# Optimization experiments

Measured on AMD Instinct MI355X. Metric: run time of the kernel, lower is better.

Reference implementation:

```python
import jax, jax.numpy as jnp
import numpy as np

NDIR = 6      # build_tree.num_directions()
IDIM = 256
ODIM = 512
B, L, NCH = 8, 4096, 8192


def setup_inputs() -> dict:
    key = jax.random.key(0)
    ks = jax.random.split(key, 9)
    last = jax.random.normal(ks[0], (B, NCH, IDIM), dtype=jnp.float32)
    child_l = jax.random.randint(ks[1], (L,), 0, NCH, dtype=jnp.int32)
    child_r = jax.random.randint(ks[2], (L,), 0, NCH, dtype=jnp.int32)
    vec = jax.random.randint(ks[3], (B, L), 0, NCH, dtype=jnp.int32)
    drev = jax.random.randint(ks[4], (NCH,), 0, 2, dtype=jnp.int32)
    dmap = jax.random.randint(ks[5], (NCH,), 0, NDIR, dtype=jnp.int32)
    # merge FC params: ndir independent Linear(2*idim -> odim) + PReLU(init=relu_weight)
    scale = 1.0 / np.sqrt(2 * IDIM)
    W_merge = jax.random.uniform(ks[6], (NDIR, ODIM, 2 * IDIM), jnp.float32, -scale, scale)
    b_merge = jax.random.uniform(ks[7], (NDIR, ODIM), jnp.float32, -scale, scale)
    alpha_merge = jnp.full((NDIR,), 0.005, dtype=jnp.float32)  # PReLU weight (relu_weight)
    return {"last": last, "W_merge": W_merge, "b_merge": b_merge,
            "alpha_merge": alpha_merge, "child_l": child_l, "child_r": child_r,
            "vec": vec, "drev": drev, "dmap": dmap}


def reference(last, W_merge, b_merge, alpha_merge, child_l, child_r, vec, drev, dmap):
    # child gathers: [B, L, idim]
    lch = last[:, child_l]
    rch = last[:, child_r]
    # per-element direction-reverse blending
    d = drev[vec][:, :, None].astype(last.dtype)          # [B, L, 1]
    a = lch * (1.0 - d) + rch * d
    b = rch * (1.0 - d) + lch * d
    ans = jnp.concatenate([a, b], axis=-1)                # [B, L, 2*idim]
    # routed merge: compute all ndir linears, then select per element (ndir is small)
    y_all = jnp.einsum('bli,doi->bldo', ans, W_merge) + b_merge   # [B, L, ndir, odim]
    dir_idx = dmap[vec]                                   # [B, L] in [0, ndir)
    y = jnp.take_along_axis(y_all, dir_idx[:, :, None, None], axis=2)[:, :, 0]  # [B, L, odim]
    alpha = alpha_merge[dir_idx][:, :, None]              # per-element PReLU slope
    return jnp.where(y > 0, y, alpha * y)
```

## Files before the change

### kernel.cpp

```cpp
#include <hip/hip_runtime.h>
#include <hip/hip_bf16.h>

#define BB 8
#define LL 4096
#define NCH 8192
#define IDIM 256
#define KDIM 512
#define ODIM 512
#define NDIR 6
#define TOT (BB * LL)

#define CAP 8192
#define IDX_OFF 64
#define ROWS_OFF (64 + 8 * CAP)
#define WS_LAST_OFF (64 + 16 * CAP)
#define LAST_ELEMS (BB * NCH * IDIM)
#define W_ELEMS (NDIR * ODIM * KDIM)
#define N_LAST8 (LAST_ELEMS / 8)
#define N_W8 (W_ELEMS / 8)

#define GEMM_CHUNK 131

typedef short short8 __attribute__((ext_vector_type(8)));
typedef float floatx4 __attribute__((ext_vector_type(4)));

__device__ inline void async_copy16(const void* g, void* l) {
  __builtin_amdgcn_global_load_lds(
      (const __attribute__((address_space(1))) void*)g,
      (__attribute__((address_space(3))) void*)l, 16, 0, 0);
}

__device__ inline void cvt8(const float* __restrict__ src,
                            __hip_bfloat16* __restrict__ dst, int i) {
  const floatx4* s = (const floatx4*)src;
  floatx4 a = s[2 * i];
  floatx4 b = s[2 * i + 1];
  union { short8 v; __hip_bfloat16 h[8]; } u;
  u.h[0] = __float2bfloat16(a[0]); u.h[1] = __float2bfloat16(a[1]);
  u.h[2] = __float2bfloat16(a[2]); u.h[3] = __float2bfloat16(a[3]);
  u.h[4] = __float2bfloat16(b[0]); u.h[5] = __float2bfloat16(b[1]);
  u.h[6] = __float2bfloat16(b[2]); u.h[7] = __float2bfloat16(b[3]);
  ((short8*)dst)[i] = u.v;
}

__global__ __launch_bounds__(256) void prep_kernel(
    const float* __restrict__ last, const float* __restrict__ W,
    const int* __restrict__ vec, const int* __restrict__ child_l,
    const int* __restrict__ child_r, const int* __restrict__ drev,
    const int* __restrict__ dmap, int* __restrict__ ws) {
  __hip_bfloat16* last_bf = (__hip_bfloat16*)(ws + WS_LAST_OFF);
  __hip_bfloat16* W_bf = last_bf + LAST_ELEMS;
  int gid = blockIdx.x * 256 + threadIdx.x;
  if (gid < N_LAST8) {
    cvt8(last, last_bf, gid);
  } else if (gid < N_LAST8 + N_W8) {
    cvt8(W, W_bf, gid - N_LAST8);
  } else {
    __shared__ int lcnt[8];
    __shared__ int gbase[8];
    int tid = threadIdx.x;
    if (tid < 8) lcnt[tid] = 0;
    __syncthreads();
    int lin = gid - (N_LAST8 + N_W8);
    int l = lin & (LL - 1);
    int v = vec[lin];
    int dir = dmap[v] & 7;
    int sw = drev[v];
    int cl = child_l[l];
    int cr = child_r[l];
    int r0 = sw ? cr : cl;
    int r1 = sw ? cl : cr;
    int pos = atomicAdd(&lcnt[dir], 1);
    __syncthreads();
    if (tid < 8) gbase[tid] = lcnt[tid] ? atomicAdd(&ws[tid], lcnt[tid]) : 0;
    __syncthreads();
    int slot = dir * CAP + gbase[dir] + pos;
    ws[IDX_OFF + slot] = lin;
    ws[ROWS_OFF + slot] = r0 | (r1 << 16);
  }
}

__global__ __launch_bounds__(256) void gemm_kernel(
    const float* __restrict__ bias, const float* __restrict__ alpha_m,
    const int* __restrict__ ws, float* __restrict__ out) {
  __shared__ __hip_bfloat16 Als[3][128 * 64];
  __shared__ __hip_bfloat16 Bls[2][128 * 64];

  int flat = blockIdx.y * 4 + blockIdx.x;
  int swz = (flat & 7) * GEMM_CHUNK + (flat >> 3);
  const int mt = swz >> 2;
  const int nt = swz & 3;

  int d = -1, count = 0, m_base = 0;
  {
    int tb = 0;
    for (int dd = 0; dd < 8; ++dd) {
      int c = ws[dd];
      int ntile = (c + 127) >> 7;
      if (mt < tb + ntile) { d = dd; count = c; m_base = (mt - tb) * 128; break; }
      tb += ntile;
    }
  }
  if (d < 0) return;

  const int* idxA = ws + IDX_OFF + d * CAP;
  const int* rowsA = ws + ROWS_OFF + d * CAP;
  const __hip_bfloat16* last_bf = (const __hip_bfloat16*)(ws + WS_LAST_OFF);
  const __hip_bfloat16* W_bf = last_bf + LAST_ELEMS;

  const int tid = threadIdx.x;
  const int wave = __builtin_amdgcn_readfirstlane(tid >> 6);
  const int lane = tid & 63;
  const int lane15 = lane & 15;
  const int quad = lane >> 4;
  const int wm = wave >> 1;
  const int wn = wave & 1;
  const int n_blk = nt * 128;

  const __hip_bfloat16* ap0[4];
  const __hip_bfloat16* ap1[4];
  const __hip_bfloat16* bp[4];
  int ldsrow[4];
#pragma unroll
  for (int i = 0; i < 4; ++i) {
    int sr = wave * 32 + i * 8 + (lane >> 3);
    ldsrow[i] = (wave * 32 + i * 8) * 64;
    int lr = m_base + sr;
    if (lr >= count) lr = count - 1;
    int lin = idxA[lr] & (TOT - 1);
    int rr = rowsA[lr];
    int b = lin >> 12;
    int r0 = rr & (NCH - 1);
    int r1 = (rr >> 16) & (NCH - 1);
    int xu = ((lane & 7) ^ (sr & 7)) * 8;
    ap0[i] = last_bf + (long long)(b * NCH + r0) * IDIM + xu;
    ap1[i] = last_bf + (long long)(b * NCH + r1) * IDIM + xu;
    bp[i] = W_bf + (long long)(d * ODIM + n_blk + sr) * KDIM + xu;
  }

#define STAGE_A(c, buf)                                              \
  {                                                                  \
    const int ko = ((c) & 3) * 64;                                   \
    _Pragma("unroll") for (int i = 0; i < 4; ++i)                    \
        async_copy16(((c) < 4 ? ap0[i] : ap1[i]) + ko,               \
                     &Als[(buf)][ldsrow[i]]);                        \
  }
#define STAGE_B(c, buf)                                              \
  {                                                                  \
    _Pragma("unroll") for (int i = 0; i < 4; ++i)                    \
        async_copy16(bp[i] + (c) * 64, &Bls[(buf)][ldsrow[i]]);      \
  }

  floatx4 acc[4][4] = {};
  const int lx = lane15 & 7;

  STAGE_B(0, 0);
  STAGE_A(0, 0);
  STAGE_A(1, 1);

#pragma unroll
  for (int c = 0; c < 8; ++c) {
    __builtin_amdgcn_s_barrier();
    if (c < 7) STAGE_B(c + 1, (c + 1) & 1);
    if (c < 6) STAGE_A(c + 2, (c + 2) % 3);
    if (c < 6) {
      asm volatile("s_waitcnt vmcnt(12)" ::: "memory");
    } else if (c == 6) {
      asm volatile("s_waitcnt vmcnt(8)" ::: "memory");
    } else {
      asm volatile("s_waitcnt vmcnt(0)" ::: "memory");
    }
    __builtin_amdgcn_sched_barrier(0);
    __builtin_amdgcn_s_barrier();

    const __hip_bfloat16* Ab = Als[c % 3];
    const __hip_bfloat16* Bb = Bls[c & 1];
#pragma unroll
    for (int s = 0; s < 2; ++s) {
      const int xcol = ((quad + 4 * s) ^ lx) * 8;
      short8 a[4], b[4];
#pragma unroll
      for (int i = 0; i < 4; ++i)
        a[i] = *(const short8*)&Ab[(wm * 64 + i * 16 + lane15) * 64 + xcol];
#pragma unroll
      for (int j = 0; j < 4; ++j)
        b[j] = *(const short8*)&Bb[(wn * 64 + j * 16 + lane15) * 64 + xcol];
#pragma unroll
      for (int i = 0; i < 4; ++i)
#pragma unroll
        for (int j = 0; j < 4; ++j)
          acc[i][j] = __builtin_amdgcn_mfma_f32_16x16x32_bf16(a[i], b[j], acc[i][j], 0, 0, 0);
    }
  }

  const float alpha = alpha_m[d];
  float bj[4];
#pragma unroll
  for (int j = 0; j < 4; ++j)
    bj[j] = bias[d * ODIM + n_blk + wn * 64 + j * 16 + lane15];

#pragma unroll
  for (int i = 0; i < 4; ++i) {
#pragma unroll
    for (int reg = 0; reg < 4; ++reg) {
      int row_id = m_base + wm * 64 + i * 16 + quad * 4 + reg;
      if (row_id >= count) continue;
      int lin = idxA[row_id] & (TOT - 1);
      float* orow = out + (long long)lin * ODIM + n_blk + wn * 64;
#pragma unroll
      for (int j = 0; j < 4; ++j) {
        float y = acc[i][j][reg] + bj[j];
        y = y > 0.f ? y : alpha * y;
        orow[j * 16 + lane15] = y;
      }
    }
  }
}

extern "C" void kernel_launch(void* const* d_in, const int* in_sizes, int n_in,
                              void* d_out, int out_size, void* d_ws, size_t ws_size,
                              hipStream_t stream) {
  const float* last = (const float*)d_in[0];
  const float* W = (const float*)d_in[1];
  const float* bias = (const float*)d_in[2];
  const float* alpha = (const float*)d_in[3];
  const int* child_l = (const int*)d_in[4];
  const int* child_r = (const int*)d_in[5];
  const int* vec = (const int*)d_in[6];
  const int* drev = (const int*)d_in[7];
  const int* dmap = (const int*)d_in[8];

  int* ws = (int*)d_ws;

  hipMemsetAsync(ws, 0, 64 * sizeof(int), stream);
  int prep_blocks = N_LAST8 / 256 + N_W8 / 256 + TOT / 256;
  prep_kernel<<<prep_blocks, 256, 0, stream>>>(last, W, vec, child_l, child_r,
                                               drev, dmap, ws);
  dim3 grid(ODIM / 128, TOT / 128 + NDIR, 1);
  gemm_kernel<<<grid, 256, 0, stream>>>(bias, alpha, ws, (float*)d_out);
}
```

Before: 164.0 us.

## Halve GEMM K-tile to 32 and raise occupancy with a new swizzled LDS layout

The GEMM K step drops from 64 to 32, so the pipeline runs 16 iterations instead of 8 and LDS buffers are halved. The kernel now asks for 4 blocks per SM via launch bounds. Global-to-LDS staging and the XOR swizzle for fragment reads are rearranged around the smaller tiles. The goal is more resident blocks to hide gather latency, at the cost of twice as many barriers and waits per tile and less MFMA work between syncs.

```diff
diff --git a/kernel.cpp b/kernel.cpp
--- a/kernel.cpp
+++ b/kernel.cpp
@@ -80,11 +80,11 @@
   }
 }
 
-__global__ __launch_bounds__(256) void gemm_kernel(
+__global__ __launch_bounds__(256, 4) void gemm_kernel(
     const float* __restrict__ bias, const float* __restrict__ alpha_m,
     const int* __restrict__ ws, float* __restrict__ out) {
-  __shared__ __hip_bfloat16 Als[3][128 * 64];
-  __shared__ __hip_bfloat16 Bls[2][128 * 64];
+  __shared__ __hip_bfloat16 Als[3][128 * 32];
+  __shared__ __hip_bfloat16 Bls[2][128 * 32];
 
   int flat = blockIdx.y * 4 + blockIdx.x;
   int swz = (flat & 7) * GEMM_CHUNK + (flat >> 3);
@@ -117,56 +117,62 @@
   const int wn = wave & 1;
   const int n_blk = nt * 128;
 
-  const __hip_bfloat16* ap0[4];
-  const __hip_bfloat16* ap1[4];
-  const __hip_bfloat16* bp[4];
-  int ldsrow[4];
-#pragma unroll
-  for (int i = 0; i < 4; ++i) {
-    int sr = wave * 32 + i * 8 + (lane >> 3);
-    ldsrow[i] = (wave * 32 + i * 8) * 64;
-    int lr = m_base + sr;
-    if (lr >= count) lr = count - 1;
-    int lin = idxA[lr] & (TOT - 1);
-    int rr = rowsA[lr];
-    int b = lin >> 12;
-    int r0 = rr & (NCH - 1);
-    int r1 = (rr >> 16) & (NCH - 1);
-    int xu = ((lane & 7) ^ (sr & 7)) * 8;
-    ap0[i] = last_bf + (long long)(b * NCH + r0) * IDIM + xu;
-    ap1[i] = last_bf + (long long)(b * NCH + r1) * IDIM + xu;
-    bp[i] = W_bf + (long long)(d * ODIM + n_blk + sr) * KDIM + xu;
-  }
-
-#define STAGE_A(c, buf)                                              \
-  {                                                                  \
-    const int ko = ((c) & 3) * 64;                                   \
-    _Pragma("unroll") for (int i = 0; i < 4; ++i)                    \
-        async_copy16(((c) < 4 ? ap0[i] : ap1[i]) + ko,               \
-                     &Als[(buf)][ldsrow[i]]);                        \
-  }
-#define STAGE_B(c, buf)                                              \
-  {                                                                  \
-    _Pragma("unroll") for (int i = 0; i < 4; ++i)                    \
-        async_copy16(bp[i] + (c) * 64, &Bls[(buf)][ldsrow[i]]);      \
+  const __hip_bfloat16* ap0[2];
+  const __hip_bfloat16* ap1[2];
+  const __hip_bfloat16* bp[2];
+  int ldsoff[2];
+  {
+    const int lp = lane >> 3;
+    const int up = (lane & 7) ^ lp;
+    const int k16e = (up & 3) * 8;
+#pragma unroll
+    for (int i = 0; i < 2; ++i) {
+      const int I = wave * 2 + i;
+      ldsoff[i] = I * 512;
+      int row_local = I * 16 + 2 * lp + (up >> 2);
+      int gr = m_base + row_local;
+      if (gr >= count) gr = count - 1;
+      int lin = idxA[gr] & (TOT - 1);
+      int rr = rowsA[gr];
+      int b = lin >> 12;
+      int r0 = rr & (NCH - 1);
+      int r1 = (rr >> 16) & (NCH - 1);
+      ap0[i] = last_bf + (long long)(b * NCH + r0) * IDIM + k16e;
+      ap1[i] = last_bf + (long long)(b * NCH + r1) * IDIM + k16e;
+      bp[i] = W_bf + (long long)(d * ODIM + n_blk + row_local) * KDIM + k16e;
+    }
+  }
+
+#define STAGE_A(c, buf)                                               \
+  {                                                                   \
+    const int ko = ((c) & 7) * 32;                                    \
+    _Pragma("unroll") for (int i = 0; i < 2; ++i)                     \
+        async_copy16(((c) < 8 ? ap0[i] : ap1[i]) + ko,                \
+                     &Als[(buf)][ldsoff[i]]);                         \
+  }
+#define STAGE_B(c, buf)                                               \
+  {                                                                   \
+    _Pragma("unroll") for (int i = 0; i < 2; ++i)                     \
+        async_copy16(bp[i] + (c) * 32, &Bls[(buf)][ldsoff[i]]);       \
   }
 
   floatx4 acc[4][4] = {};
-  const int lx = lane15 & 7;
+  const int t3 = lane15 >> 1;
+  const int col8 = (((lane15 & 1) * 4 + quad) ^ t3) * 8;
 
   STAGE_B(0, 0);
   STAGE_A(0, 0);
   STAGE_A(1, 1);
 
 #pragma unroll
-  for (int c = 0; c < 8; ++c) {
+  for (int c = 0; c < 16; ++c) {
     __builtin_amdgcn_s_barrier();
-    if (c < 7) STAGE_B(c + 1, (c + 1) & 1);
-    if (c < 6) STAGE_A(c + 2, (c + 2) % 3);
-    if (c < 6) {
-      asm volatile("s_waitcnt vmcnt(12)" ::: "memory");
-    } else if (c == 6) {
-      asm volatile("s_waitcnt vmcnt(8)" ::: "memory");
+    if (c < 15) STAGE_B(c + 1, (c + 1) & 1);
+    if (c < 14) STAGE_A(c + 2, (c + 2) % 3);
+    if (c < 14) {
+      asm volatile("s_waitcnt vmcnt(6)" ::: "memory");
+    } else if (c == 14) {
+      asm volatile("s_waitcnt vmcnt(4)" ::: "memory");
     } else {
       asm volatile("s_waitcnt vmcnt(0)" ::: "memory");
     }
@@ -175,22 +181,18 @@
 
     const __hip_bfloat16* Ab = Als[c % 3];
     const __hip_bfloat16* Bb = Bls[c & 1];
-#pragma unroll
-    for (int s = 0; s < 2; ++s) {
-      const int xcol = ((quad + 4 * s) ^ lx) * 8;
-      short8 a[4], b[4];
-#pragma unroll
-      for (int i = 0; i < 4; ++i)
-        a[i] = *(const short8*)&Ab[(wm * 64 + i * 16 + lane15) * 64 + xcol];
+    short8 a[4], b[4];
+#pragma unroll
+    for (int i = 0; i < 4; ++i)
+      a[i] = *(const short8*)&Ab[(wm * 32 + i * 8 + t3) * 64 + col8];
+#pragma unroll
+    for (int j = 0; j < 4; ++j)
+      b[j] = *(const short8*)&Bb[(wn * 32 + j * 8 + t3) * 64 + col8];
+#pragma unroll
+    for (int i = 0; i < 4; ++i)
 #pragma unroll
       for (int j = 0; j < 4; ++j)
-        b[j] = *(const short8*)&Bb[(wn * 64 + j * 16 + lane15) * 64 + xcol];
-#pragma unroll
-      for (int i = 0; i < 4; ++i)
-#pragma unroll
-        for (int j = 0; j < 4; ++j)
-          acc[i][j] = __builtin_amdgcn_mfma_f32_16x16x32_bf16(a[i], b[j], acc[i][j], 0, 0, 0);
-    }
+        acc[i][j] = __builtin_amdgcn_mfma_f32_16x16x32_bf16(a[i], b[j], acc[i][j], 0, 0, 0);
   }
 
   const float alpha = alpha_m[d];
```

Result: no change. 163.3 us (-0.5%).
